# Kernel tuning notes

Measured on AMD Instinct MI355X. Metric: run time of the kernel, lower is better.

Reference implementation:

```python
import jax, jax.numpy as jnp
import numpy as np

N = 50000
E = 600000
D = 128
HEADS = 4
G = 64  # num graphs
EPS = 1e-5


def setup_inputs() -> dict:
    key = jax.random.key(0)
    ks = jax.random.split(key, 16)
    s = 0.05
    inp = {
        'x': jax.random.normal(ks[0], (N, D), jnp.float32),
        'edge_index': jax.random.randint(ks[1], (2, E), 0, N, jnp.int64),
        'batch': jnp.sort(jax.random.randint(ks[2], (N,), 0, G, jnp.int64)),
        # GCN layer 1
        'W1': jax.random.normal(ks[3], (D, D), jnp.float32) * s,
        'b1': jnp.zeros((D,), jnp.float32),
        'g1': jnp.ones((D,), jnp.float32),
        'beta1': jnp.zeros((D,), jnp.float32),
        # GCN layer 2
        'W2': jax.random.normal(ks[4], (D, D), jnp.float32) * s,
        'b2': jnp.zeros((D,), jnp.float32),
        'g2': jnp.ones((D,), jnp.float32),
        'beta2': jnp.zeros((D,), jnp.float32),
        # GAT (heads=4, concat=False -> mean over heads)
        'gat_W': jax.random.normal(ks[5], (D, HEADS * D), jnp.float32) * s,
        'att_src': jax.random.normal(ks[6], (HEADS, D), jnp.float32) * s,
        'att_dst': jax.random.normal(ks[7], (HEADS, D), jnp.float32) * s,
        'gat_b': jnp.zeros((D,), jnp.float32),
    }
    return inp


def _layer_norm(x, g, b):
    mu = jnp.mean(x, axis=-1, keepdims=True)
    var = jnp.mean((x - mu) ** 2, axis=-1, keepdims=True)
    return (x - mu) * jax.lax.rsqrt(var + EPS) * g + b


def _gcn(x, W, b, src, dst, deg_inv_sqrt):
    h = x @ W                                    # [N, D]
    norm = deg_inv_sqrt[src] * deg_inv_sqrt[dst]  # [E']
    msg = norm[:, None] * h[src]                 # [E', D] gather
    return jax.ops.segment_sum(msg, dst, num_segments=N) + b


def _gat(x, W, b, att_src, att_dst, src, dst):
    h = (x @ W).reshape(N, HEADS, D)             # [N, H, D]
    a_s = jnp.einsum('nhd,hd->nh', h, att_src)   # [N, H]
    a_d = jnp.einsum('nhd,hd->nh', h, att_dst)
    e = jax.nn.leaky_relu(a_s[src] + a_d[dst], 0.2)          # [E', H]
    m = jax.ops.segment_max(e, dst, num_segments=N)          # segment softmax
    ex = jnp.exp(e - m[dst])
    den = jax.ops.segment_sum(ex, dst, num_segments=N)
    alpha = ex / den[dst]                                     # [E', H]
    out = jax.ops.segment_sum(alpha[:, :, None] * h[src], dst, num_segments=N)
    return jnp.mean(out, axis=1) + b             # concat=False -> head mean


def reference(x, edge_index, batch, W1, b1, g1, beta1, W2, b2, g2, beta2,
              gat_W, gat_b, att_src, att_dst):
    # add self loops (PyG default for GCNConv and GATConv)
    loops = jnp.arange(N, dtype=edge_index.dtype)
    src = jnp.concatenate([edge_index[0], loops])
    dst = jnp.concatenate([edge_index[1], loops])
    deg = jax.ops.segment_sum(jnp.ones_like(dst, jnp.float32), dst, num_segments=N)
    deg_inv_sqrt = jnp.where(deg > 0, jax.lax.rsqrt(jnp.maximum(deg, 1.0)), 0.0)

    # GCN stack: conv -> LayerNorm -> relu -> dropout(eval=identity)
    h = jax.nn.relu(_layer_norm(_gcn(x, W1, b1, src, dst, deg_inv_sqrt), g1, beta1))
    h = jax.nn.relu(_layer_norm(_gcn(h, W2, b2, src, dst, deg_inv_sqrt), g2, beta2))

    h = jax.nn.relu(_gat(h, gat_W, gat_b, att_src, att_dst, src, dst))
    node_embeddings = h

    cnt = jax.ops.segment_sum(jnp.ones((N,), jnp.float32), batch, num_segments=G)
    mean_pool = jax.ops.segment_sum(h, batch, num_segments=G) / jnp.maximum(cnt, 1.0)[:, None]
    max_pool = jax.ops.segment_max(h, batch, num_segments=G)
    graph_embedding = jnp.concatenate([mean_pool, max_pool], axis=1)  # [G, 2D]
    return graph_embedding, node_embeddings
```

## Files before the change

kernel.cpp:

```cpp
#include <hip/hip_runtime.h>
#include <math.h>


#define TPB 256

typedef __attribute__((ext_vector_type(8))) short short8;
typedef __attribute__((ext_vector_type(4))) float f32x4;
union U4S8 { uint4 u; short8 s; };

__device__ __forceinline__ float lrelu(float x) { return x > 0.f ? x : 0.2f * x; }

__device__ __forceinline__ unsigned short f2bf(float f) {
    unsigned int u = __float_as_uint(f);
    u += 0x7fffu + ((u >> 16) & 1u);
    return (unsigned short)(u >> 16);
}
__device__ __forceinline__ float2 bf2x(unsigned int u) {
    return make_float2(__uint_as_float(u << 16), __uint_as_float(u & 0xffff0000u));
}
__device__ __forceinline__ float sel4(float4 v, int h) {
    float r = v.x;
    r = (h == 1) ? v.y : r;
    r = (h == 2) ? v.z : r;
    r = (h == 3) ? v.w : r;
    return r;
}

__global__ __launch_bounds__(TPB) void k_hist(const int* __restrict__ dst,
                                              int* __restrict__ deg, int e) {
    int i = blockIdx.x * TPB + threadIdx.x;
    if (i < e) atomicAdd(&deg[dst[i]], 1);
}

__global__ __launch_bounds__(TPB) void k_scan_part(const int* __restrict__ deg,
                                                   int* __restrict__ part, int n) {
    int i = blockIdx.x * TPB + threadIdx.x;
    int v = (i < n) ? deg[i] : 0;
#pragma unroll
    for (int o = 32; o > 0; o >>= 1) v += __shfl_xor(v, o);
    __shared__ int sw[4];
    if ((threadIdx.x & 63) == 0) sw[threadIdx.x >> 6] = v;
    __syncthreads();
    if (threadIdx.x == 0) part[blockIdx.x] = sw[0] + sw[1] + sw[2] + sw[3];
}

__global__ __launch_bounds__(TPB) void k_scan_top(int* __restrict__ part, int nb) {
    __shared__ int sm[TPB];
    int t = threadIdx.x;
    int v = (t < nb) ? part[t] : 0;
    sm[t] = v;
    __syncthreads();
    for (int off = 1; off < TPB; off <<= 1) {
        int u = (t >= off) ? sm[t - off] : 0;
        __syncthreads();
        sm[t] += u;
        __syncthreads();
    }
    if (t < nb) part[t] = sm[t] - v;
}

__global__ __launch_bounds__(TPB) void k_scan_apply(const int* __restrict__ deg,
                                                    const int* __restrict__ part,
                                                    int* __restrict__ row_start,
                                                    int* __restrict__ cursor,
                                                    float* __restrict__ dis,
                                                    int n, int e_total) {
    __shared__ int sm[TPB];
    int i = blockIdx.x * TPB + threadIdx.x;
    int t = threadIdx.x;
    int d = (i < n) ? deg[i] : 0;
    sm[t] = d;
    __syncthreads();
    for (int off = 1; off < TPB; off <<= 1) {
        int u = (t >= off) ? sm[t - off] : 0;
        __syncthreads();
        sm[t] += u;
        __syncthreads();
    }
    if (i < n) {
        int rs = part[blockIdx.x] + sm[t] - d;
        row_start[i] = rs;
        cursor[i] = rs;
        dis[i] = rsqrtf((float)(d + 1));
    }
    if (blockIdx.x == 0 && t == 0) row_start[n] = e_total;
}

__global__ __launch_bounds__(TPB) void k_scatter(const int* __restrict__ src,
                                                 const int* __restrict__ dst,
                                                 int* __restrict__ cursor,
                                                 int* __restrict__ csr_src, int e) {
    int i = blockIdx.x * TPB + threadIdx.x;
    if (i < e) {
        int p = atomicAdd(&cursor[dst[i]], 1);
        csr_src[p] = src[i];
    }
}

__global__ __launch_bounds__(TPB) void k_f2bf(const float* __restrict__ in,
                                              unsigned short* __restrict__ out, int n4) {
    int i = blockIdx.x * TPB + threadIdx.x;
    if (i >= n4) return;
    float4 v = ((const float4*)in)[i];
    unsigned int p0 = (unsigned int)f2bf(v.x) | ((unsigned int)f2bf(v.y) << 16);
    unsigned int p1 = (unsigned int)f2bf(v.z) | ((unsigned int)f2bf(v.w) << 16);
    ((uint2*)out)[i] = make_uint2(p0, p1);
}

__global__ __launch_bounds__(TPB) void k_wt(const float* __restrict__ W,
                                            unsigned short* __restrict__ Wt, int ocols) {
    int i = blockIdx.x * TPB + threadIdx.x;
    if (i >= 128 * ocols) return;
    int k = i / ocols, n = i - k * ocols;
    Wt[n * 128 + k] = f2bf(W[i]);
}

__global__ __launch_bounds__(TPB, 2) void k_gemm_mfma(const unsigned short* __restrict__ feat,
                                                      const unsigned short* __restrict__ Wt,
                                                      unsigned short* __restrict__ C,
                                                      int nrows, int ocols) {
    __shared__ uint4 wl[2048];
    int t = threadIdx.x;
    int cb = blockIdx.y << 7;
#pragma unroll
    for (int i = 0; i < 8; ++i) {
        int fi = i * 256 + t;
        int l = fi & 63, ct = (fi >> 6) & 7, ks = fi >> 9;
        int chan = cb + ct * 16 + (l & 15);
        wl[fi] = ((const uint4*)(Wt + (size_t)chan * 128))[ks * 4 + (l >> 4)];
    }
    __syncthreads();

    int wave = t >> 6, lane = t & 63;
    int wr = wave >> 1, wc = wave & 1;
    int nbase = (blockIdx.x << 7) + (wc << 6);
    const uint4* brow[4];
#pragma unroll
    for (int nt = 0; nt < 4; ++nt) {
        int node = nbase + nt * 16 + (lane & 15);
        node = node < nrows ? node : (nrows - 1);
        brow[nt] = (const uint4*)(feat + (size_t)node * 128);
    }
    f32x4 acc[4][4];
#pragma unroll
    for (int mt = 0; mt < 4; ++mt)
#pragma unroll
        for (int nt = 0; nt < 4; ++nt) acc[mt][nt] = (f32x4)0.f;

    int kq = lane >> 4;
#pragma unroll
    for (int ks = 0; ks < 4; ++ks) {
        U4S8 a[4], b[4];
#pragma unroll
        for (int mt = 0; mt < 4; ++mt)
            a[mt].u = wl[(ks * 8 + wr * 4 + mt) * 64 + lane];
#pragma unroll
        for (int nt = 0; nt < 4; ++nt)
            b[nt].u = brow[nt][ks * 4 + kq];
#pragma unroll
        for (int mt = 0; mt < 4; ++mt)
#pragma unroll
            for (int nt = 0; nt < 4; ++nt)
                acc[mt][nt] = __builtin_amdgcn_mfma_f32_16x16x32_bf16(
                    a[mt].s, b[nt].s, acc[mt][nt], 0, 0, 0);
    }
#pragma unroll
    for (int nt = 0; nt < 4; ++nt) {
        int node = nbase + nt * 16 + (lane & 15);
        if (node >= nrows) continue;
#pragma unroll
        for (int mt = 0; mt < 4; ++mt) {
            int chan = cb + (wr << 6) + mt * 16 + (lane >> 4) * 4;
            f32x4 v = acc[mt][nt];
            unsigned int p0 = (unsigned int)f2bf(v.x) | ((unsigned int)f2bf(v.y) << 16);
            unsigned int p1 = (unsigned int)f2bf(v.z) | ((unsigned int)f2bf(v.w) << 16);
            *(uint2*)(C + (size_t)node * ocols + chan) = make_uint2(p0, p1);
        }
    }
}

__global__ __launch_bounds__(TPB) void k_gcn_fused(const unsigned short* __restrict__ hb,
                                                   const int* __restrict__ csr_src,
                                                   const int* __restrict__ row_start,
                                                   const float* __restrict__ dis,
                                                   const float* __restrict__ b,
                                                   const float* __restrict__ g,
                                                   const float* __restrict__ beta,
                                                   unsigned short* __restrict__ out, int n) {
    __shared__ int   ssrc[4][64];
    __shared__ float swt[4][64];
    int node = (blockIdx.x * TPB + threadIdx.x) >> 6;
    int lane = threadIdx.x & 63;
    int wid = threadIdx.x >> 6;
    if (node >= n) return;
    int s0 = row_start[node], s1 = row_start[node + 1];
    float dn = dis[node];
    const uint4* hq = (const uint4*)hb;
    int q = lane >> 4, fl = lane & 15;
    float acc[8];
#pragma unroll
    for (int i = 0; i < 8; ++i) acc[i] = 0.f;
    for (int base = s0; base < s1; base += 64) {
        int cnt = min(64, s1 - base);
        int sidx = 0; float w = 0.f;
        if (lane < cnt) { sidx = csr_src[base + lane]; w = dis[sidx]; }
        ssrc[wid][lane] = sidx;
        swt[wid][lane] = w;
        for (int j = 0; j < cnt; j += 4) {
            int jj = j + q;
            int ok = jj < cnt;
            int s = ssrc[wid][ok ? jj : 0];
            float wj = ok ? swt[wid][jj] : 0.f;
            uint4 u = hq[(size_t)s * 16 + fl];
            float2 p0 = bf2x(u.x), p1 = bf2x(u.y), p2 = bf2x(u.z), p3 = bf2x(u.w);
            acc[0] += wj * p0.x; acc[1] += wj * p0.y;
            acc[2] += wj * p1.x; acc[3] += wj * p1.y;
            acc[4] += wj * p2.x; acc[5] += wj * p2.y;
            acc[6] += wj * p3.x; acc[7] += wj * p3.y;
        }
    }
#pragma unroll
    for (int i = 0; i < 8; ++i) {
        acc[i] += __shfl_xor(acc[i], 16);
        acc[i] += __shfl_xor(acc[i], 32);
    }
    float sl = dn * dn;
    uint4 us = hq[(size_t)node * 16 + fl];
    float2 h0 = bf2x(us.x), h1 = bf2x(us.y), h2 = bf2x(us.z), h3 = bf2x(us.w);
    float4 b0 = ((const float4*)b)[fl * 2], b1 = ((const float4*)b)[fl * 2 + 1];
    float v[8];
    v[0] = dn * acc[0] + sl * h0.x + b0.x;
    v[1] = dn * acc[1] + sl * h0.y + b0.y;
    v[2] = dn * acc[2] + sl * h1.x + b0.z;
    v[3] = dn * acc[3] + sl * h1.y + b0.w;
    v[4] = dn * acc[4] + sl * h2.x + b1.x;
    v[5] = dn * acc[5] + sl * h2.y + b1.y;
    v[6] = dn * acc[6] + sl * h3.x + b1.z;
    v[7] = dn * acc[7] + sl * h3.y + b1.w;
    float s = 0.f, sq = 0.f;
#pragma unroll
    for (int i = 0; i < 8; ++i) { s += v[i]; sq += v[i] * v[i]; }
#pragma unroll
    for (int o = 8; o > 0; o >>= 1) {
        s  += __shfl_xor(s, o);
        sq += __shfl_xor(sq, o);
    }
    float mu = s * (1.f / 128.f);
    float var = sq * (1.f / 128.f) - mu * mu;
    float rstd = rsqrtf(var + 1e-5f);
    float4 g0  = ((const float4*)g)[fl * 2],    g1v = ((const float4*)g)[fl * 2 + 1];
    float4 bt0 = ((const float4*)beta)[fl * 2], bt1 = ((const float4*)beta)[fl * 2 + 1];
    float o0 = fmaxf((v[0] - mu) * rstd * g0.x + bt0.x, 0.f);
    float o1 = fmaxf((v[1] - mu) * rstd * g0.y + bt0.y, 0.f);
    float o2 = fmaxf((v[2] - mu) * rstd * g0.z + bt0.z, 0.f);
    float o3 = fmaxf((v[3] - mu) * rstd * g0.w + bt0.w, 0.f);
    float o4 = fmaxf((v[4] - mu) * rstd * g1v.x + bt1.x, 0.f);
    float o5 = fmaxf((v[5] - mu) * rstd * g1v.y + bt1.y, 0.f);
    float o6 = fmaxf((v[6] - mu) * rstd * g1v.z + bt1.z, 0.f);
    float o7 = fmaxf((v[7] - mu) * rstd * g1v.w + bt1.w, 0.f);
    if (q == 0) {
        uint4 pk;
        pk.x = (unsigned int)f2bf(o0) | ((unsigned int)f2bf(o1) << 16);
        pk.y = (unsigned int)f2bf(o2) | ((unsigned int)f2bf(o3) << 16);
        pk.z = (unsigned int)f2bf(o4) | ((unsigned int)f2bf(o5) << 16);
        pk.w = (unsigned int)f2bf(o6) | ((unsigned int)f2bf(o7) << 16);
        ((uint4*)out)[(size_t)node * 16 + fl] = pk;
    }
}

__global__ __launch_bounds__(TPB) void k_att_dots(const unsigned short* __restrict__ hgb,
                                                  const float* __restrict__ att_s,
                                                  const float* __restrict__ att_d,
                                                  float* __restrict__ a_s,
                                                  float* __restrict__ a_d, int n) {
    int wave = (blockIdx.x * TPB + threadIdx.x) >> 6;
    int lane = threadIdx.x & 63;
    if (wave >= n) return;
    int h = lane >> 4, j = lane & 15;
    const uint4* hq = (const uint4*)hgb;
    uint4 u = hq[(size_t)wave * 64 + lane];
    float2 p0 = bf2x(u.x), p1 = bf2x(u.y), p2 = bf2x(u.z), p3 = bf2x(u.w);
    const float4* s4 = (const float4*)(att_s + h * 128 + j * 8);
    const float4* d4 = (const float4*)(att_d + h * 128 + j * 8);
    float4 s0 = s4[0], s1 = s4[1];
    float4 d0 = d4[0], d1 = d4[1];
    float ps = p0.x * s0.x + p0.y * s0.y + p1.x * s0.z + p1.y * s0.w
             + p2.x * s1.x + p2.y * s1.y + p3.x * s1.z + p3.y * s1.w;
    float pd = p0.x * d0.x + p0.y * d0.y + p1.x * d0.z + p1.y * d0.w
             + p2.x * d1.x + p2.y * d1.y + p3.x * d1.z + p3.y * d1.w;
#pragma unroll
    for (int o = 8; o > 0; o >>= 1) {
        ps += __shfl_xor(ps, o);
        pd += __shfl_xor(pd, o);
    }
    if (j == 0) {
        a_s[wave * 4 + h] = ps;
        a_d[wave * 4 + h] = pd;
    }
}

__global__ __launch_bounds__(TPB) void k_gat_fused(const unsigned short* __restrict__ hgb,
                                                   const float* __restrict__ a_s,
                                                   const float* __restrict__ a_d,
                                                   const int* __restrict__ csr_src,
                                                   const int* __restrict__ row_start,
                                                   const float* __restrict__ gat_b,
                                                   float* __restrict__ node_out, int n) {
    __shared__ int   ssrc[4][64];
    __shared__ float swt[4][4][65];
    int node = (blockIdx.x * TPB + threadIdx.x) >> 6;
    int lane = threadIdx.x & 63;
    int wid = threadIdx.x >> 6;
    if (node >= n) return;
    int s0 = row_start[node], s1 = row_start[node + 1];
    int h = lane >> 4;
    const float4* as4 = (const float4*)a_s;
    float4 ad = ((const float4*)a_d)[node];
    float4 asn = as4[node];
    float4 wself;
    wself.x = __expf(lrelu(asn.x + ad.x));
    wself.y = __expf(lrelu(asn.y + ad.y));
    wself.z = __expf(lrelu(asn.z + ad.z));
    wself.w = __expf(lrelu(asn.w + ad.w));
    const uint4* hq = (const uint4*)hgb;
    float acc[8];
    {
        float wsh = sel4(wself, h);
        uint4 u = hq[(size_t)node * 64 + lane];
        float2 p0 = bf2x(u.x), p1 = bf2x(u.y), p2 = bf2x(u.z), p3 = bf2x(u.w);
        acc[0] = wsh * p0.x; acc[1] = wsh * p0.y;
        acc[2] = wsh * p1.x; acc[3] = wsh * p1.y;
        acc[4] = wsh * p2.x; acc[5] = wsh * p2.y;
        acc[6] = wsh * p3.x; acc[7] = wsh * p3.y;
    }
    float4 den = make_float4(0.f, 0.f, 0.f, 0.f);
    for (int base = s0; base < s1; base += 64) {
        int cnt = min(64, s1 - base);
        int sidx = 0;
        float4 w4 = make_float4(0.f, 0.f, 0.f, 0.f);
        if (lane < cnt) {
            sidx = csr_src[base + lane];
            float4 a = as4[sidx];
            w4.x = __expf(lrelu(a.x + ad.x));
            w4.y = __expf(lrelu(a.y + ad.y));
            w4.z = __expf(lrelu(a.z + ad.z));
            w4.w = __expf(lrelu(a.w + ad.w));
            den.x += w4.x; den.y += w4.y; den.z += w4.z; den.w += w4.w;
        }
        ssrc[wid][lane] = sidx;
        swt[wid][0][lane] = w4.x;
        swt[wid][1][lane] = w4.y;
        swt[wid][2][lane] = w4.z;
        swt[wid][3][lane] = w4.w;
        int j = 0;
        for (; j + 4 <= cnt; j += 4) {
            int sa = ssrc[wid][j + 0], sb = ssrc[wid][j + 1];
            int sc = ssrc[wid][j + 2], sd = ssrc[wid][j + 3];
            float wa = swt[wid][h][j + 0], wb = swt[wid][h][j + 1];
            float wc = swt[wid][h][j + 2], wd = swt[wid][h][j + 3];
            uint4 ua = hq[(size_t)sa * 64 + lane];
            uint4 ub = hq[(size_t)sb * 64 + lane];
            uint4 uc = hq[(size_t)sc * 64 + lane];
            uint4 ud = hq[(size_t)sd * 64 + lane];
            float2 p0, p1, p2, p3;
            p0 = bf2x(ua.x); p1 = bf2x(ua.y); p2 = bf2x(ua.z); p3 = bf2x(ua.w);
            acc[0] += wa * p0.x; acc[1] += wa * p0.y; acc[2] += wa * p1.x; acc[3] += wa * p1.y;
            acc[4] += wa * p2.x; acc[5] += wa * p2.y; acc[6] += wa * p3.x; acc[7] += wa * p3.y;
            p0 = bf2x(ub.x); p1 = bf2x(ub.y); p2 = bf2x(ub.z); p3 = bf2x(ub.w);
            acc[0] += wb * p0.x; acc[1] += wb * p0.y; acc[2] += wb * p1.x; acc[3] += wb * p1.y;
            acc[4] += wb * p2.x; acc[5] += wb * p2.y; acc[6] += wb * p3.x; acc[7] += wb * p3.y;
            p0 = bf2x(uc.x); p1 = bf2x(uc.y); p2 = bf2x(uc.z); p3 = bf2x(uc.w);
            acc[0] += wc * p0.x; acc[1] += wc * p0.y; acc[2] += wc * p1.x; acc[3] += wc * p1.y;
            acc[4] += wc * p2.x; acc[5] += wc * p2.y; acc[6] += wc * p3.x; acc[7] += wc * p3.y;
            p0 = bf2x(ud.x); p1 = bf2x(ud.y); p2 = bf2x(ud.z); p3 = bf2x(ud.w);
            acc[0] += wd * p0.x; acc[1] += wd * p0.y; acc[2] += wd * p1.x; acc[3] += wd * p1.y;
            acc[4] += wd * p2.x; acc[5] += wd * p2.y; acc[6] += wd * p3.x; acc[7] += wd * p3.y;
        }
        for (; j < cnt; ++j) {
            int s = ssrc[wid][j];
            float wj = swt[wid][h][j];
            uint4 u = hq[(size_t)s * 64 + lane];
            float2 p0 = bf2x(u.x), p1 = bf2x(u.y), p2 = bf2x(u.z), p3 = bf2x(u.w);
            acc[0] += wj * p0.x; acc[1] += wj * p0.y;
            acc[2] += wj * p1.x; acc[3] += wj * p1.y;
            acc[4] += wj * p2.x; acc[5] += wj * p2.y;
            acc[6] += wj * p3.x; acc[7] += wj * p3.y;
        }
    }
#pragma unroll
    for (int o = 32; o > 0; o >>= 1) {
        den.x += __shfl_xor(den.x, o);
        den.y += __shfl_xor(den.y, o);
        den.z += __shfl_xor(den.z, o);
        den.w += __shfl_xor(den.w, o);
    }
    den.x += wself.x; den.y += wself.y; den.z += wself.z; den.w += wself.w;
    float winv = 0.25f / sel4(den, h);
#pragma unroll
    for (int j = 0; j < 8; ++j) acc[j] *= winv;
#pragma unroll
    for (int j = 0; j < 8; ++j) acc[j] += __shfl_xor(acc[j], 16);
#pragma unroll
    for (int j = 0; j < 8; ++j) acc[j] += __shfl_xor(acc[j], 32);
    int fl = lane & 15;
    float4 gb0 = ((const float4*)gat_b)[fl * 2], gb1 = ((const float4*)gat_b)[fl * 2 + 1];
    if (lane < 16) {
        float4* o4 = (float4*)(node_out + (size_t)node * 128 + fl * 8);
        o4[0] = make_float4(fmaxf(acc[0] + gb0.x, 0.f), fmaxf(acc[1] + gb0.y, 0.f),
                            fmaxf(acc[2] + gb0.z, 0.f), fmaxf(acc[3] + gb0.w, 0.f));
        o4[1] = make_float4(fmaxf(acc[4] + gb1.x, 0.f), fmaxf(acc[5] + gb1.y, 0.f),
                            fmaxf(acc[6] + gb1.z, 0.f), fmaxf(acc[7] + gb1.w, 0.f));
    }
}

__global__ __launch_bounds__(TPB) void k_pool(const float* __restrict__ node_out,
                                              const int* __restrict__ batch,
                                              float* __restrict__ mean_acc,
                                              float* __restrict__ max_acc,
                                              float* __restrict__ cnt, int n) {
    int wave = (blockIdx.x * TPB + threadIdx.x) >> 6;
    int lane = threadIdx.x & 63;
    int n0 = wave * 16;
    if (n0 >= n) return;
    int n1 = min(n0 + 16, n);
    float2 bsum = make_float2(0.f, 0.f), bmax = make_float2(0.f, 0.f);
    int cur_g = batch[n0];
    int cntloc = 0;
    for (int nn = n0; nn < n1; ++nn) {
        int g = batch[nn];
        if (g != cur_g) {
            float* ma = mean_acc + cur_g * 128 + lane * 2;
            atomicAdd(ma + 0, bsum.x);
            atomicAdd(ma + 1, bsum.y);
            int* mxp = (int*)(max_acc + cur_g * 128 + lane * 2);
            atomicMax(mxp + 0, __float_as_int(bmax.x));
            atomicMax(mxp + 1, __float_as_int(bmax.y));
            if (lane == 0) atomicAdd(&cnt[cur_g], (float)cntloc);
            bsum = make_float2(0.f, 0.f);
            bmax = make_float2(0.f, 0.f);
            cntloc = 0;
            cur_g = g;
        }
        float2 o = ((const float2*)node_out)[(size_t)nn * 64 + lane];
        bsum.x += o.x; bsum.y += o.y;
        bmax.x = fmaxf(bmax.x, o.x); bmax.y = fmaxf(bmax.y, o.y);
        ++cntloc;
    }
    float* ma = mean_acc + cur_g * 128 + lane * 2;
    atomicAdd(ma + 0, bsum.x);
    atomicAdd(ma + 1, bsum.y);
    int* mxp = (int*)(max_acc + cur_g * 128 + lane * 2);
    atomicMax(mxp + 0, __float_as_int(bmax.x));
    atomicMax(mxp + 1, __float_as_int(bmax.y));
    if (lane == 0) atomicAdd(&cnt[cur_g], (float)cntloc);
}

__global__ __launch_bounds__(TPB) void k_pool_final(const float* __restrict__ mean_acc,
                                                    const float* __restrict__ max_acc,
                                                    const float* __restrict__ cnt,
                                                    float* __restrict__ gout, int g128) {
    int i = blockIdx.x * TPB + threadIdx.x;
    if (i >= g128) return;
    int g = i >> 7, d = i & 127;
    float c = fmaxf(cnt[g], 1.f);
    gout[g * 256 + d] = mean_acc[i] / c;
    gout[g * 256 + 128 + d] = max_acc[i];
}

extern "C" void kernel_launch(void* const* d_in, const int* in_sizes, int n_in,
                              void* d_out, int out_size, void* d_ws, size_t ws_size,
                              hipStream_t stream) {
    const float* x       = (const float*)d_in[0];
    const int*   ei      = (const int*)d_in[1];
    const int*   batch   = (const int*)d_in[2];
    const float* W1      = (const float*)d_in[3];
    const float* b1      = (const float*)d_in[4];
    const float* g1      = (const float*)d_in[5];
    const float* beta1   = (const float*)d_in[6];
    const float* W2      = (const float*)d_in[7];
    const float* b2      = (const float*)d_in[8];
    const float* g2      = (const float*)d_in[9];
    const float* beta2   = (const float*)d_in[10];
    const float* gat_W   = (const float*)d_in[11];
    const float* att_src = (const float*)d_in[12];
    const float* att_dst = (const float*)d_in[13];
    const float* gat_b   = (const float*)d_in[14];

    const int N = in_sizes[0] / 128;
    const int E = in_sizes[1] / 2;
    const int G = (out_size - N * 128) / 256;
    const int* src = ei;
    const int* dst = ei + E;

    float* ws = (float*)d_ws;
    float* dis      = ws; ws += N;
    float* a_s      = ws; ws += N * 4;
    float* a_d      = ws; ws += N * 4;
    float* mean_acc = ws; ws += G * 128;
    float* max_acc  = ws; ws += G * 128;
    float* cnt      = ws; ws += G;
    unsigned short* xb  = (unsigned short*)ws; ws += (size_t)N * 64;
    unsigned short* Hbf = (unsigned short*)ws; ws += (size_t)N * 64;
    unsigned short* Bbf = (unsigned short*)ws; ws += (size_t)N * 64;
    unsigned short* Cbf = (unsigned short*)ws; ws += (size_t)N * 64;
    unsigned short* hgb = (unsigned short*)ws; ws += (size_t)N * 256;
    unsigned short* Wt1 = (unsigned short*)ws; ws += 128 * 64;
    unsigned short* Wt2 = (unsigned short*)ws; ws += 128 * 64;
    unsigned short* Wtg = (unsigned short*)ws; ws += 512 * 64;
    int* deg       = (int*)ws; ws += N;
    int* part      = (int*)ws; ws += 256;
    int* row_start = (int*)ws; ws += N + 1;
    int* cursor    = (int*)ws; ws += N + 1;
    int* csr_src   = (int*)ws; ws += E;

    float* gout = (float*)d_out;
    float* node_out = gout + G * 256;

    auto cdiv = [](long a, long b) { return (int)((a + b - 1) / b); };
    const int nb = cdiv(N, TPB);

    hipMemsetAsync(deg, 0, (size_t)N * 4, stream);
    k_hist<<<cdiv(E, TPB), TPB, 0, stream>>>(dst, deg, E);
    k_scan_part<<<nb, TPB, 0, stream>>>(deg, part, N);
    k_scan_top<<<1, TPB, 0, stream>>>(part, nb);
    k_scan_apply<<<nb, TPB, 0, stream>>>(deg, part, row_start, cursor, dis, N, E);
    k_scatter<<<cdiv(E, TPB), TPB, 0, stream>>>(src, dst, cursor, csr_src, E);

    k_f2bf<<<cdiv((long)N * 32, TPB), TPB, 0, stream>>>(x, xb, N * 32);
    k_wt<<<cdiv(128 * 128, TPB), TPB, 0, stream>>>(W1, Wt1, 128);
    k_wt<<<cdiv(128 * 128, TPB), TPB, 0, stream>>>(W2, Wt2, 128);
    k_wt<<<cdiv(128 * 512, TPB), TPB, 0, stream>>>(gat_W, Wtg, 512);

    k_gemm_mfma<<<dim3(cdiv(N, 128), 1), TPB, 0, stream>>>(xb, Wt1, Hbf, N, 128);
    k_gcn_fused<<<cdiv((long)N * 64, TPB), TPB, 0, stream>>>(Hbf, csr_src, row_start, dis,
                                                             b1, g1, beta1, Bbf, N);
    k_gemm_mfma<<<dim3(cdiv(N, 128), 1), TPB, 0, stream>>>(Bbf, Wt2, Hbf, N, 128);
    k_gcn_fused<<<cdiv((long)N * 64, TPB), TPB, 0, stream>>>(Hbf, csr_src, row_start, dis,
                                                             b2, g2, beta2, Cbf, N);
    k_gemm_mfma<<<dim3(cdiv(N, 128), 4), TPB, 0, stream>>>(Cbf, Wtg, hgb, N, 512);
    k_att_dots<<<cdiv((long)N * 64, TPB), TPB, 0, stream>>>(hgb, att_src, att_dst, a_s, a_d, N);
    k_gat_fused<<<cdiv((long)N * 64, TPB), TPB, 0, stream>>>(hgb, a_s, a_d, csr_src, row_start,
                                                             gat_b, node_out, N);

    hipMemsetAsync(mean_acc, 0, (size_t)(G * 256 + G) * 4, stream);
    k_pool<<<cdiv((long)cdiv(N, 16) * 64, TPB), TPB, 0, stream>>>(node_out, batch,
                                                                  mean_acc, max_acc, cnt, N);
    k_pool_final<<<cdiv((long)G * 128, TPB), TPB, 0, stream>>>(mean_acc, max_acc, cnt, gout, G * 128);
}
```

Baseline: 455.3 us.

## Fuse input conversion, weight transposes, and attention dots into GEMMs; unroll GCN gather

The first GEMM now reads fp32 node features directly and converts them to bf16 in registers, which removes the separate conversion kernel and its intermediate buffer. The three weight-transpose launches are merged into one kernel. The GAT attention dot products are computed from the fp32 GEMM accumulators and reduced through shared-memory atomics, replacing the kernel that re-read the bf16 hgb tensor. The GCN gather loop is unrolled by two to keep more independent loads in flight, at the cost of extra registers and slightly different rounding in the attention logits.

```diff
diff --git a/kernel.cpp b/kernel.cpp
--- a/kernel.cpp
+++ b/kernel.cpp
@@ -24,6 +24,9 @@
     r = (h == 2) ? v.z : r;
     r = (h == 3) ? v.w : r;
     return r;
+}
+__device__ __forceinline__ float dot4(f32x4 a, float4 b) {
+    return a.x * b.x + a.y * b.y + a.z * b.z + a.w * b.w;
 }
 
 __global__ __launch_bounds__(TPB) void k_hist(const int* __restrict__ dst,
@@ -97,29 +100,37 @@
     }
 }
 
-__global__ __launch_bounds__(TPB) void k_f2bf(const float* __restrict__ in,
-                                              unsigned short* __restrict__ out, int n4) {
+__global__ __launch_bounds__(TPB) void k_wt_all(const float* __restrict__ W1,
+                                                const float* __restrict__ W2,
+                                                const float* __restrict__ Wg,
+                                                unsigned short* __restrict__ Wt1,
+                                                unsigned short* __restrict__ Wt2,
+                                                unsigned short* __restrict__ Wtg) {
     int i = blockIdx.x * TPB + threadIdx.x;
-    if (i >= n4) return;
-    float4 v = ((const float4*)in)[i];
-    unsigned int p0 = (unsigned int)f2bf(v.x) | ((unsigned int)f2bf(v.y) << 16);
-    unsigned int p1 = (unsigned int)f2bf(v.z) | ((unsigned int)f2bf(v.w) << 16);
-    ((uint2*)out)[i] = make_uint2(p0, p1);
-}
-
-__global__ __launch_bounds__(TPB) void k_wt(const float* __restrict__ W,
-                                            unsigned short* __restrict__ Wt, int ocols) {
-    int i = blockIdx.x * TPB + threadIdx.x;
-    if (i >= 128 * ocols) return;
-    int k = i / ocols, n = i - k * ocols;
-    Wt[n * 128 + k] = f2bf(W[i]);
+    if (i < 16384) {
+        int k = i >> 7, n = i & 127;
+        Wt1[n * 128 + k] = f2bf(W1[i]);
+    } else if (i < 32768) {
+        int j = i - 16384;
+        int k = j >> 7, n = j & 127;
+        Wt2[n * 128 + k] = f2bf(W2[j]);
+    } else if (i < 98304) {
+        int j = i - 32768;
+        int k = j >> 9, n = j & 511;
+        Wtg[n * 128 + k] = f2bf(Wg[j]);
+    }
 }
 
 __global__ __launch_bounds__(TPB, 2) void k_gemm_mfma(const unsigned short* __restrict__ feat,
                                                       const unsigned short* __restrict__ Wt,
                                                       unsigned short* __restrict__ C,
-                                                      int nrows, int ocols) {
+                                                      int nrows, int ocols,
+                                                      const float* __restrict__ att_s,
+                                                      const float* __restrict__ att_d,
+                                                      float* __restrict__ a_s,
+                                                      float* __restrict__ a_d) {
     __shared__ uint4 wl[2048];
+    __shared__ float sas[128], sad[128];
     int t = threadIdx.x;
     int cb = blockIdx.y << 7;
 #pragma unroll
@@ -157,6 +168,112 @@
 #pragma unroll
         for (int nt = 0; nt < 4; ++nt)
             b[nt].u = brow[nt][ks * 4 + kq];
+#pragma unroll
+        for (int mt = 0; mt < 4; ++mt)
+#pragma unroll
+            for (int nt = 0; nt < 4; ++nt)
+                acc[mt][nt] = __builtin_amdgcn_mfma_f32_16x16x32_bf16(
+                    a[mt].s, b[nt].s, acc[mt][nt], 0, 0, 0);
+    }
+#pragma unroll
+    for (int nt = 0; nt < 4; ++nt) {
+        int node = nbase + nt * 16 + (lane & 15);
+        if (node >= nrows) continue;
+#pragma unroll
+        for (int mt = 0; mt < 4; ++mt) {
+            int chan = cb + (wr << 6) + mt * 16 + (lane >> 4) * 4;
+            f32x4 v = acc[mt][nt];
+            unsigned int p0 = (unsigned int)f2bf(v.x) | ((unsigned int)f2bf(v.y) << 16);
+            unsigned int p1 = (unsigned int)f2bf(v.z) | ((unsigned int)f2bf(v.w) << 16);
+            *(uint2*)(C + (size_t)node * ocols + chan) = make_uint2(p0, p1);
+        }
+    }
+    if (att_s) {
+        if (t < 128) { sas[t] = 0.f; sad[t] = 0.f; }
+        __syncthreads();
+        int h = blockIdx.y;
+        float4 asv[4], adv[4];
+#pragma unroll
+        for (int mt = 0; mt < 4; ++mt) {
+            int cbase = h * 128 + (wr << 6) + mt * 16 + (lane >> 4) * 4;
+            asv[mt] = *(const float4*)(att_s + cbase);
+            adv[mt] = *(const float4*)(att_d + cbase);
+        }
+#pragma unroll
+        for (int nt = 0; nt < 4; ++nt) {
+            float ds = 0.f, dd = 0.f;
+#pragma unroll
+            for (int mt = 0; mt < 4; ++mt) {
+                ds += dot4(acc[mt][nt], asv[mt]);
+                dd += dot4(acc[mt][nt], adv[mt]);
+            }
+            ds += __shfl_xor(ds, 16); ds += __shfl_xor(ds, 32);
+            dd += __shfl_xor(dd, 16); dd += __shfl_xor(dd, 32);
+            if (lane < 16) {
+                atomicAdd(&sas[(wc << 6) + nt * 16 + lane], ds);
+                atomicAdd(&sad[(wc << 6) + nt * 16 + lane], dd);
+            }
+        }
+        __syncthreads();
+        if (t < 128) {
+            int node = (blockIdx.x << 7) + t;
+            if (node < nrows) a_s[node * 4 + h] = sas[t];
+        } else {
+            int t2 = t - 128;
+            int node = (blockIdx.x << 7) + t2;
+            if (node < nrows) a_d[node * 4 + h] = sad[t2];
+        }
+    }
+}
+
+__global__ __launch_bounds__(TPB, 2) void k_gemm_mfma_f32(const float* __restrict__ feat,
+                                                          const unsigned short* __restrict__ Wt,
+                                                          unsigned short* __restrict__ C,
+                                                          int nrows, int ocols) {
+    __shared__ uint4 wl[2048];
+    int t = threadIdx.x;
+    int cb = blockIdx.y << 7;
+#pragma unroll
+    for (int i = 0; i < 8; ++i) {
+        int fi = i * 256 + t;
+        int l = fi & 63, ct = (fi >> 6) & 7, ks = fi >> 9;
+        int chan = cb + ct * 16 + (l & 15);
+        wl[fi] = ((const uint4*)(Wt + (size_t)chan * 128))[ks * 4 + (l >> 4)];
+    }
+    __syncthreads();
+
+    int wave = t >> 6, lane = t & 63;
+    int wr = wave >> 1, wc = wave & 1;
+    int nbase = (blockIdx.x << 7) + (wc << 6);
+    const float4* brow[4];
+#pragma unroll
+    for (int nt = 0; nt < 4; ++nt) {
+        int node = nbase + nt * 16 + (lane & 15);
+        node = node < nrows ? node : (nrows - 1);
+        brow[nt] = (const float4*)(feat + (size_t)node * 128);
+    }
+    f32x4 acc[4][4];
+#pragma unroll
+    for (int mt = 0; mt < 4; ++mt)
+#pragma unroll
+        for (int nt = 0; nt < 4; ++nt) acc[mt][nt] = (f32x4)0.f;
+
+    int kq = lane >> 4;
+#pragma unroll
+    for (int ks = 0; ks < 4; ++ks) {
+        U4S8 a[4], b[4];
+#pragma unroll
+        for (int mt = 0; mt < 4; ++mt)
+            a[mt].u = wl[(ks * 8 + wr * 4 + mt) * 64 + lane];
+#pragma unroll
+        for (int nt = 0; nt < 4; ++nt) {
+            float4 f0 = brow[nt][ks * 8 + kq * 2];
+            float4 f1 = brow[nt][ks * 8 + kq * 2 + 1];
+            b[nt].u.x = (unsigned int)f2bf(f0.x) | ((unsigned int)f2bf(f0.y) << 16);
+            b[nt].u.y = (unsigned int)f2bf(f0.z) | ((unsigned int)f2bf(f0.w) << 16);
+            b[nt].u.z = (unsigned int)f2bf(f1.x) | ((unsigned int)f2bf(f1.y) << 16);
+            b[nt].u.w = (unsigned int)f2bf(f1.z) | ((unsigned int)f2bf(f1.w) << 16);
+        }
 #pragma unroll
         for (int mt = 0; mt < 4; ++mt)
 #pragma unroll
@@ -206,17 +323,25 @@
         if (lane < cnt) { sidx = csr_src[base + lane]; w = dis[sidx]; }
         ssrc[wid][lane] = sidx;
         swt[wid][lane] = w;
-        for (int j = 0; j < cnt; j += 4) {
-            int jj = j + q;
-            int ok = jj < cnt;
-            int s = ssrc[wid][ok ? jj : 0];
-            float wj = ok ? swt[wid][jj] : 0.f;
-            uint4 u = hq[(size_t)s * 16 + fl];
-            float2 p0 = bf2x(u.x), p1 = bf2x(u.y), p2 = bf2x(u.z), p3 = bf2x(u.w);
-            acc[0] += wj * p0.x; acc[1] += wj * p0.y;
-            acc[2] += wj * p1.x; acc[3] += wj * p1.y;
-            acc[4] += wj * p2.x; acc[5] += wj * p2.y;
-            acc[6] += wj * p3.x; acc[7] += wj * p3.y;
+        for (int j = 0; j < cnt; j += 8) {
+            int j0 = j + q, j1 = j + 4 + q;
+            int ok0 = j0 < cnt, ok1 = j1 < cnt;
+            int sA = ssrc[wid][ok0 ? j0 : 0];
+            int sB = ssrc[wid][ok1 ? j1 : 0];
+            float wA = ok0 ? swt[wid][j0] : 0.f;
+            float wB = ok1 ? swt[wid][j1] : 0.f;
+            uint4 uA = hq[(size_t)sA * 16 + fl];
+            uint4 uB = hq[(size_t)sB * 16 + fl];
+            float2 p0 = bf2x(uA.x), p1 = bf2x(uA.y), p2 = bf2x(uA.z), p3 = bf2x(uA.w);
+            acc[0] += wA * p0.x; acc[1] += wA * p0.y;
+            acc[2] += wA * p1.x; acc[3] += wA * p1.y;
+            acc[4] += wA * p2.x; acc[5] += wA * p2.y;
+            acc[6] += wA * p3.x; acc[7] += wA * p3.y;
+            p0 = bf2x(uB.x); p1 = bf2x(uB.y); p2 = bf2x(uB.z); p3 = bf2x(uB.w);
+            acc[0] += wB * p0.x; acc[1] += wB * p0.y;
+            acc[2] += wB * p1.x; acc[3] += wB * p1.y;
+            acc[4] += wB * p2.x; acc[5] += wB * p2.y;
+            acc[6] += wB * p3.x; acc[7] += wB * p3.y;
         }
     }
 #pragma unroll
@@ -265,37 +390,6 @@
         pk.z = (unsigned int)f2bf(o4) | ((unsigned int)f2bf(o5) << 16);
         pk.w = (unsigned int)f2bf(o6) | ((unsigned int)f2bf(o7) << 16);
         ((uint4*)out)[(size_t)node * 16 + fl] = pk;
-    }
-}
-
-__global__ __launch_bounds__(TPB) void k_att_dots(const unsigned short* __restrict__ hgb,
-                                                  const float* __restrict__ att_s,
-                                                  const float* __restrict__ att_d,
-                                                  float* __restrict__ a_s,
-                                                  float* __restrict__ a_d, int n) {
-    int wave = (blockIdx.x * TPB + threadIdx.x) >> 6;
-    int lane = threadIdx.x & 63;
-    if (wave >= n) return;
-    int h = lane >> 4, j = lane & 15;
-    const uint4* hq = (const uint4*)hgb;
-    uint4 u = hq[(size_t)wave * 64 + lane];
-    float2 p0 = bf2x(u.x), p1 = bf2x(u.y), p2 = bf2x(u.z), p3 = bf2x(u.w);
-    const float4* s4 = (const float4*)(att_s + h * 128 + j * 8);
-    const float4* d4 = (const float4*)(att_d + h * 128 + j * 8);
-    float4 s0 = s4[0], s1 = s4[1];
-    float4 d0 = d4[0], d1 = d4[1];
-    float ps = p0.x * s0.x + p0.y * s0.y + p1.x * s0.z + p1.y * s0.w
-             + p2.x * s1.x + p2.y * s1.y + p3.x * s1.z + p3.y * s1.w;
-    float pd = p0.x * d0.x + p0.y * d0.y + p1.x * d0.z + p1.y * d0.w
-             + p2.x * d1.x + p2.y * d1.y + p3.x * d1.z + p3.y * d1.w;
-#pragma unroll
-    for (int o = 8; o > 0; o >>= 1) {
-        ps += __shfl_xor(ps, o);
-        pd += __shfl_xor(pd, o);
-    }
-    if (j == 0) {
-        a_s[wave * 4 + h] = ps;
-        a_d[wave * 4 + h] = pd;
     }
 }
 
@@ -499,7 +593,6 @@
     float* mean_acc = ws; ws += G * 128;
     float* max_acc  = ws; ws += G * 128;
     float* cnt      = ws; ws += G;
-    unsigned short* xb  = (unsigned short*)ws; ws += (size_t)N * 64;
     unsigned short* Hbf = (unsigned short*)ws; ws += (size_t)N * 64;
     unsigned short* Bbf = (unsigned short*)ws; ws += (size_t)N * 64;
     unsigned short* Cbf = (unsigned short*)ws; ws += (size_t)N * 64;
@@ -526,19 +619,17 @@
     k_scan_apply<<<nb, TPB, 0, stream>>>(deg, part, row_start, cursor, dis, N, E);
     k_scatter<<<cdiv(E, TPB), TPB, 0, stream>>>(src, dst, cursor, csr_src, E);
 
-    k_f2bf<<<cdiv((long)N * 32, TPB), TPB, 0, stream>>>(x, xb, N * 32);
-    k_wt<<<cdiv(128 * 128, TPB), TPB, 0, stream>>>(W1, Wt1, 128);
-    k_wt<<<cdiv(128 * 128, TPB), TPB, 0, stream>>>(W2, Wt2, 128);
-    k_wt<<<cdiv(128 * 512, TPB), TPB, 0, stream>>>(gat_W, Wtg, 512);
-
-    k_gemm_mfma<<<dim3(cdiv(N, 128), 1), TPB, 0, stream>>>(xb, Wt1, Hbf, N, 128);
+    k_wt_all<<<cdiv(98304, TPB), TPB, 0, stream>>>(W1, W2, gat_W, Wt1, Wt2, Wtg);
+
+    k_gemm_mfma_f32<<<dim3(cdiv(N, 128), 1), TPB, 0, stream>>>(x, Wt1, Hbf, N, 128);
     k_gcn_fused<<<cdiv((long)N * 64, TPB), TPB, 0, stream>>>(Hbf, csr_src, row_start, dis,
                                                              b1, g1, beta1, Bbf, N);
-    k_gemm_mfma<<<dim3(cdiv(N, 128), 1), TPB, 0, stream>>>(Bbf, Wt2, Hbf, N, 128);
+    k_gemm_mfma<<<dim3(cdiv(N, 128), 1), TPB, 0, stream>>>(Bbf, Wt2, Hbf, N, 128,
+                                                           nullptr, nullptr, nullptr, nullptr);
     k_gcn_fused<<<cdiv((long)N * 64, TPB), TPB, 0, stream>>>(Hbf, csr_src, row_start, dis,
                                                              b2, g2, beta2, Cbf, N);
-    k_gemm_mfma<<<dim3(cdiv(N, 128), 4), TPB, 0, stream>>>(Cbf, Wtg, hgb, N, 512);
-    k_att_dots<<<cdiv((long)N * 64, TPB), TPB, 0, stream>>>(hgb, att_src, att_dst, a_s, a_d, N);
+    k_gemm_mfma<<<dim3(cdiv(N, 128), 4), TPB, 0, stream>>>(Cbf, Wtg, hgb, N, 512,
+                                                           att_src, att_dst, a_s, a_d);
     k_gat_fused<<<cdiv((long)N * 64, TPB), TPB, 0, stream>>>(hgb, a_s, a_d, csr_src, row_start,
                                                              gat_b, node_out, N);
 
```

After: 432.0 us. 1.05x faster.
